# Performance work log

Hardware: AMD Instinct MI355X
Metric: run time of the kernel (lower is better)

## Reference

```python
import jax, jax.numpy as jnp
import numpy as np

DEPTH = 11  # tree depth -> depth+1 routing steps, n_nodes = 2**(DEPTH+1)-1 = 4095


def setup_inputs() -> dict:
    key = jax.random.key(0)
    k1, k2, k3 = jax.random.split(key, 3)
    B, D_in, D_out = 8192, 2048, 2048
    n_nodes = 2 ** (DEPTH + 1) - 1
    x = jax.random.normal(k1, (B, D_in), dtype=jnp.float32)
    # nn.Linear(input_width, n_nodes, bias=False).weight : (n_nodes, D_in)
    W_in = jax.random.normal(k2, (n_nodes, D_in), dtype=jnp.float32) / np.sqrt(D_in).astype(np.float32)
    # nn.Linear(n_nodes, output_width, bias=False).weight : (D_out, n_nodes)
    W_out = jax.random.normal(k3, (D_out, n_nodes), dtype=jnp.float32) / np.sqrt(n_nodes).astype(np.float32)
    return {"x": x, "W_in": W_in, "W_out": W_out}


def reference(x, W_in, W_out):
    B = x.shape[0]
    # Torch loop recomputes linear_in(x) every step; the result is identical each
    # iteration, so compute the (B, n_nodes) logits once and gather per depth step.
    logits_all = x @ W_in.T  # (B, n_nodes)

    def step(cur, _):
        # gather the logit of each sample's current tree node
        score = jnp.take_along_axis(logits_all, cur[:, None], axis=1)[:, 0]  # (B,)
        nxt = cur * 2 + (score >= 0).astype(jnp.int32) + 1  # left/right child
        return nxt, (cur, score)

    init = jnp.zeros((B,), dtype=jnp.int32)
    _, (nodes, scores) = jax.lax.scan(step, init, None, length=DEPTH + 1)
    nodes = nodes.T    # (B, depth+1) visited node ids
    scores = scores.T  # (B, depth+1) selected logits

    mlp1 = jax.nn.gelu(scores, approximate=False)  # exact GELU, matches nn.GELU
    # Conditional output projection: only the depth+1 visited columns of W_out
    # contribute per sample (FFF / conditional-MoE semantics).
    W_sel = W_out.T[nodes]  # (B, depth+1, D_out)
    return jnp.einsum('bd,bdo->bo', mlp1, W_sel)
```

## Files before the change

kernel.cpp:

```cpp
#include <hip/hip_runtime.h>
#include <math.h>

#define B_SZ     8192
#define D_IN     2048
#define D_OUT    2048
#define N_NODES  4095
#define STEPS    12
#define N_LEAVES 2048
#define N_SUB    512
#define CAP      64

typedef float f4_t __attribute__((ext_vector_type(4)));

__device__ __forceinline__ float4 nt_load4(const float* p) {
  f4_t v = __builtin_nontemporal_load((const f4_t*)p);
  return make_float4(v.x, v.y, v.z, v.w);
}
__device__ __forceinline__ void nt_store4(float* p, float4 v) {
  f4_t t; t.x = v.x; t.y = v.y; t.z = v.z; t.w = v.w;
  __builtin_nontemporal_store(t, (f4_t*)p);
}

__global__ __launch_bounds__(256) void transpose_wout(
    const float* __restrict__ W, float* __restrict__ Wt) {
  __shared__ float tile[64][65];
  const int bx = blockIdx.x;
  const int tid = threadIdx.x;
  const int col0 = (bx & 63) * 64;
  const int row0 = (bx >> 6) * 64;
  const int r  = tid >> 4;
  const int c4 = (tid & 15) * 4;

  #pragma unroll
  for (int i = 0; i < 4; ++i) {
    const int row = r + i * 16;
    const float* src = W + (size_t)(row0 + row) * N_NODES + col0 + c4;
    if (col0 + c4 + 3 < N_NODES) {
      const float4 v = nt_load4(src);
      tile[c4 + 0][row] = v.x; tile[c4 + 1][row] = v.y;
      tile[c4 + 2][row] = v.z; tile[c4 + 3][row] = v.w;
    } else {
      #pragma unroll
      for (int k = 0; k < 4; ++k)
        tile[c4 + k][row] = (col0 + c4 + k < N_NODES) ? src[k] : 0.0f;
    }
  }
  __syncthreads();
  #pragma unroll
  for (int i = 0; i < 4; ++i) {
    const int rn = r + i * 16;
    const int node = col0 + rn;
    if (node < N_NODES) {
      float4 v;
      v.x = tile[rn][c4 + 0]; v.y = tile[rn][c4 + 1];
      v.z = tile[rn][c4 + 2]; v.w = tile[rn][c4 + 3];
      *(float4*)(Wt + (size_t)node * D_OUT + row0 + c4) = v;
    }
  }
}

__global__ __launch_bounds__(256) void route_kernel(
    const float* __restrict__ x, const float* __restrict__ W_in,
    int* __restrict__ cnt, int* __restrict__ bucket,
    float* __restrict__ gsc) {
  const int wave = (int)((blockIdx.x * (size_t)blockDim.x + threadIdx.x) >> 6);
  const int lane = threadIdx.x & 63;
  if (wave >= B_SZ) return;

  const float* xbase = x + (size_t)wave * D_IN;
  float4 xv[8];
  #pragma unroll
  for (int i = 0; i < 8; ++i) xv[i] = nt_load4(xbase + (lane + i * 64) * 4);

  int cur = 0;
  #pragma unroll
  for (int d = 0; d < STEPS; ++d) {
    const float4* wr = (const float4*)(W_in + (size_t)cur * D_IN);
    float s = 0.0f;
    #pragma unroll
    for (int i = 0; i < 8; ++i) {
      const float4 w = wr[lane + i * 64];
      s += xv[i].x * w.x + xv[i].y * w.y + xv[i].z * w.z + xv[i].w * w.w;
    }
    #pragma unroll
    for (int off = 32; off > 0; off >>= 1) s += __shfl_xor(s, off);

    if (lane == 0) {
      gsc[wave * STEPS + d] = 0.5f * s * (1.0f + erff(s * 0.70710678118654752f));
      if (d == STEPS - 1) {
        const int leaf = cur - 2047;
        const int pos = atomicAdd(&cnt[leaf], 1);
        if (pos < CAP) bucket[leaf * CAP + pos] = wave;
      }
    }
    cur = cur * 2 + ((s >= 0.0f) ? 2 : 1);
  }
}

__global__ __launch_bounds__(256) void out_kernel(
    const float* __restrict__ Wt, const int* __restrict__ cnt,
    const int* __restrict__ bucket, const float* __restrict__ gsc,
    float* __restrict__ out) {
  const int sub = blockIdx.x * 4 + (threadIdx.x >> 6);
  const int lane = threadIdx.x & 63;
  const int col = blockIdx.y * 256 + lane * 4;

  int anc[10];
  {
    int nd = 511 + sub;
    #pragma unroll
    for (int d = 9; d >= 0; --d) { anc[d] = nd; nd = (nd - 1) >> 1; }
  }
  const int p10a = 1023 + 2 * sub;
  const int leaf0n = 2047 + 4 * sub;

  float4 wa[10], wp[2], wl[4];
  #pragma unroll
  for (int d = 0; d < 10; ++d)
    wa[d] = *(const float4*)(Wt + (size_t)anc[d] * D_OUT + col);
  #pragma unroll
  for (int k = 0; k < 2; ++k)
    wp[k] = *(const float4*)(Wt + (size_t)(p10a + k) * D_OUT + col);
  #pragma unroll
  for (int k = 0; k < 4; ++k)
    wl[k] = *(const float4*)(Wt + (size_t)(leaf0n + k) * D_OUT + col);

  int n0 = cnt[4 * sub + 0]; if (n0 > CAP) n0 = CAP;
  int n1 = cnt[4 * sub + 1]; if (n1 > CAP) n1 = CAP;
  int n2 = cnt[4 * sub + 2]; if (n2 > CAP) n2 = CAP;
  int n3 = cnt[4 * sub + 3]; if (n3 > CAP) n3 = CAP;
  const int p1 = n0, p2 = n0 + n1, p3 = n0 + n1 + n2;
  const int total = p3 + n3;

  for (int base = 0; base < total; base += 64) {
    const int m = (total - base < 64) ? (total - base) : 64;
    int packed = 0;
    {
      const int gi = base + lane;
      if (gi < total) {
        int lc, off;
        if      (gi < p1) { lc = 0; off = 0;  }
        else if (gi < p2) { lc = 1; off = p1; }
        else if (gi < p3) { lc = 2; off = p2; }
        else              { lc = 3; off = p3; }
        const int b = bucket[(4 * sub + lc) * CAP + (gi - off)];
        packed = (lc << 28) | b;
      }
    }
    int pA = __shfl(packed, 0);
    int pB = __shfl(packed, (m > 1) ? 1 : 0);
    const float4* gA = (const float4*)(gsc + (size_t)(pA & 0x0FFFFFFF) * STEPS);
    float4 a0 = gA[0], a1 = gA[1], a2 = gA[2];
    const float4* gB = (const float4*)(gsc + (size_t)(pB & 0x0FFFFFFF) * STEPS);
    float4 b0 = gB[0], b1 = gB[1], b2 = gB[2];

    for (int j = 0; j < m; ++j) {
      int jn = j + 2; if (jn >= m) jn = m - 1;
      const int pC = __shfl(packed, jn);
      const float4* gC = (const float4*)(gsc + (size_t)(pC & 0x0FFFFFFF) * STEPS);
      const float4 t0 = gC[0], t1 = gC[1], t2 = gC[2];

      const int b  = pA & 0x0FFFFFFF;
      const int lc = pA >> 28;
      const float4 w10 = (lc & 2) ? wp[1] : wp[0];
      const float4 w11 = (lc & 2) ? ((lc & 1) ? wl[3] : wl[2])
                                  : ((lc & 1) ? wl[1] : wl[0]);
      float4 acc;
      acc.x = a0.x * wa[0].x; acc.y = a0.x * wa[0].y;
      acc.z = a0.x * wa[0].z; acc.w = a0.x * wa[0].w;
      acc.x += a0.y * wa[1].x; acc.y += a0.y * wa[1].y;
      acc.z += a0.y * wa[1].z; acc.w += a0.y * wa[1].w;
      acc.x += a0.z * wa[2].x; acc.y += a0.z * wa[2].y;
      acc.z += a0.z * wa[2].z; acc.w += a0.z * wa[2].w;
      acc.x += a0.w * wa[3].x; acc.y += a0.w * wa[3].y;
      acc.z += a0.w * wa[3].z; acc.w += a0.w * wa[3].w;
      acc.x += a1.x * wa[4].x; acc.y += a1.x * wa[4].y;
      acc.z += a1.x * wa[4].z; acc.w += a1.x * wa[4].w;
      acc.x += a1.y * wa[5].x; acc.y += a1.y * wa[5].y;
      acc.z += a1.y * wa[5].z; acc.w += a1.y * wa[5].w;
      acc.x += a1.z * wa[6].x; acc.y += a1.z * wa[6].y;
      acc.z += a1.z * wa[6].z; acc.w += a1.z * wa[6].w;
      acc.x += a1.w * wa[7].x; acc.y += a1.w * wa[7].y;
      acc.z += a1.w * wa[7].z; acc.w += a1.w * wa[7].w;
      acc.x += a2.x * wa[8].x; acc.y += a2.x * wa[8].y;
      acc.z += a2.x * wa[8].z; acc.w += a2.x * wa[8].w;
      acc.x += a2.y * wa[9].x; acc.y += a2.y * wa[9].y;
      acc.z += a2.y * wa[9].z; acc.w += a2.y * wa[9].w;
      acc.x += a2.z * w10.x;   acc.y += a2.z * w10.y;
      acc.z += a2.z * w10.z;   acc.w += a2.z * w10.w;
      acc.x += a2.w * w11.x;   acc.y += a2.w * w11.y;
      acc.z += a2.w * w11.z;   acc.w += a2.w * w11.w;
      nt_store4(out + (size_t)b * D_OUT + col, acc);

      pA = pB; a0 = b0; a1 = b1; a2 = b2;
      pB = pC; b0 = t0; b1 = t1; b2 = t2;
    }
  }
}

extern "C" void kernel_launch(void* const* d_in, const int* in_sizes, int n_in,
                              void* d_out, int out_size, void* d_ws, size_t ws_size,
                              hipStream_t stream) {
  const float* x     = (const float*)d_in[0];
  const float* W_in  = (const float*)d_in[1];
  const float* W_out = (const float*)d_in[2];
  float* out = (float*)d_out;

  char* p = (char*)d_ws;
  float* Wt     = (float*)p;  p += (size_t)N_NODES * D_OUT * sizeof(float);
  int*   cnt    = (int*)p;    p += (size_t)N_LEAVES * sizeof(int);
  int*   bucket = (int*)p;    p += (size_t)N_LEAVES * CAP * sizeof(int);
  float* gsc    = (float*)p;

  hipMemsetAsync(cnt, 0, (size_t)N_LEAVES * sizeof(int), stream);

  route_kernel<<<dim3(B_SZ / 4), dim3(256), 0, stream>>>(
      x, W_in, cnt, bucket, gsc);

  transpose_wout<<<dim3(2048), dim3(256), 0, stream>>>(W_out, Wt);

  out_kernel<<<dim3(N_SUB / 4, 8), dim3(256), 0, stream>>>(
      Wt, cnt, bucket, gsc, out);
}
```

Measured before the change: 232.8 us.

## Split output kernel to one column per lane and hoist route weight loads

The output kernel now gives each lane one scalar column instead of a float4 and launches four times as many column blocks. This raises parallelism and cuts per-thread register pressure, but every sample's score row is reloaded by four times as many waves and stores become scalar. The routing kernel's loops are manually unrolled so all eight W_in float4 loads are issued before the dot product, exposing more memory-level parallelism per step.

```diff
diff --git a/kernel.cpp b/kernel.cpp
--- a/kernel.cpp
+++ b/kernel.cpp
@@ -15,10 +15,6 @@
 __device__ __forceinline__ float4 nt_load4(const float* p) {
   f4_t v = __builtin_nontemporal_load((const f4_t*)p);
   return make_float4(v.x, v.y, v.z, v.w);
-}
-__device__ __forceinline__ void nt_store4(float* p, float4 v) {
-  f4_t t; t.x = v.x; t.y = v.y; t.z = v.z; t.w = v.w;
-  __builtin_nontemporal_store(t, (f4_t*)p);
 }
 
 __global__ __launch_bounds__(256) void transpose_wout(
@@ -68,20 +64,37 @@
   if (wave >= B_SZ) return;
 
   const float* xbase = x + (size_t)wave * D_IN;
-  float4 xv[8];
-  #pragma unroll
-  for (int i = 0; i < 8; ++i) xv[i] = nt_load4(xbase + (lane + i * 64) * 4);
+  float4 xv0 = nt_load4(xbase + (lane + 0 * 64) * 4);
+  float4 xv1 = nt_load4(xbase + (lane + 1 * 64) * 4);
+  float4 xv2 = nt_load4(xbase + (lane + 2 * 64) * 4);
+  float4 xv3 = nt_load4(xbase + (lane + 3 * 64) * 4);
+  float4 xv4 = nt_load4(xbase + (lane + 4 * 64) * 4);
+  float4 xv5 = nt_load4(xbase + (lane + 5 * 64) * 4);
+  float4 xv6 = nt_load4(xbase + (lane + 6 * 64) * 4);
+  float4 xv7 = nt_load4(xbase + (lane + 7 * 64) * 4);
 
   int cur = 0;
   #pragma unroll
   for (int d = 0; d < STEPS; ++d) {
     const float4* wr = (const float4*)(W_in + (size_t)cur * D_IN);
+    const float4 w0 = wr[lane + 0 * 64];
+    const float4 w1 = wr[lane + 1 * 64];
+    const float4 w2 = wr[lane + 2 * 64];
+    const float4 w3 = wr[lane + 3 * 64];
+    const float4 w4 = wr[lane + 4 * 64];
+    const float4 w5 = wr[lane + 5 * 64];
+    const float4 w6 = wr[lane + 6 * 64];
+    const float4 w7 = wr[lane + 7 * 64];
     float s = 0.0f;
-    #pragma unroll
-    for (int i = 0; i < 8; ++i) {
-      const float4 w = wr[lane + i * 64];
-      s += xv[i].x * w.x + xv[i].y * w.y + xv[i].z * w.z + xv[i].w * w.w;
-    }
+    s += xv0.x * w0.x + xv0.y * w0.y + xv0.z * w0.z + xv0.w * w0.w;
+    s += xv1.x * w1.x + xv1.y * w1.y + xv1.z * w1.z + xv1.w * w1.w;
+    s += xv2.x * w2.x + xv2.y * w2.y + xv2.z * w2.z + xv2.w * w2.w;
+    s += xv3.x * w3.x + xv3.y * w3.y + xv3.z * w3.z + xv3.w * w3.w;
+    s += xv4.x * w4.x + xv4.y * w4.y + xv4.z * w4.z + xv4.w * w4.w;
+    s += xv5.x * w5.x + xv5.y * w5.y + xv5.z * w5.z + xv5.w * w5.w;
+    s += xv6.x * w6.x + xv6.y * w6.y + xv6.z * w6.z + xv6.w * w6.w;
+    s += xv7.x * w7.x + xv7.y * w7.y + xv7.z * w7.z + xv7.w * w7.w;
+
     #pragma unroll
     for (int off = 32; off > 0; off >>= 1) s += __shfl_xor(s, off);
 
@@ -103,7 +116,7 @@
     float* __restrict__ out) {
   const int sub = blockIdx.x * 4 + (threadIdx.x >> 6);
   const int lane = threadIdx.x & 63;
-  const int col = blockIdx.y * 256 + lane * 4;
+  const int col = blockIdx.y * 64 + lane;
 
   int anc[10];
   {
@@ -114,16 +127,16 @@
   const int p10a = 1023 + 2 * sub;
   const int leaf0n = 2047 + 4 * sub;
 
-  float4 wa[10], wp[2], wl[4];
+  float wa[10], wp[2], wl[4];
   #pragma unroll
   for (int d = 0; d < 10; ++d)
-    wa[d] = *(const float4*)(Wt + (size_t)anc[d] * D_OUT + col);
+    wa[d] = Wt[(size_t)anc[d] * D_OUT + col];
   #pragma unroll
   for (int k = 0; k < 2; ++k)
-    wp[k] = *(const float4*)(Wt + (size_t)(p10a + k) * D_OUT + col);
+    wp[k] = Wt[(size_t)(p10a + k) * D_OUT + col];
   #pragma unroll
   for (int k = 0; k < 4; ++k)
-    wl[k] = *(const float4*)(Wt + (size_t)(leaf0n + k) * D_OUT + col);
+    wl[k] = Wt[(size_t)(leaf0n + k) * D_OUT + col];
 
   int n0 = cnt[4 * sub + 0]; if (n0 > CAP) n0 = CAP;
   int n1 = cnt[4 * sub + 1]; if (n1 > CAP) n1 = CAP;
@@ -162,35 +175,23 @@
 
       const int b  = pA & 0x0FFFFFFF;
       const int lc = pA >> 28;
-      const float4 w10 = (lc & 2) ? wp[1] : wp[0];
-      const float4 w11 = (lc & 2) ? ((lc & 1) ? wl[3] : wl[2])
-                                  : ((lc & 1) ? wl[1] : wl[0]);
-      float4 acc;
-      acc.x = a0.x * wa[0].x; acc.y = a0.x * wa[0].y;
-      acc.z = a0.x * wa[0].z; acc.w = a0.x * wa[0].w;
-      acc.x += a0.y * wa[1].x; acc.y += a0.y * wa[1].y;
-      acc.z += a0.y * wa[1].z; acc.w += a0.y * wa[1].w;
-      acc.x += a0.z * wa[2].x; acc.y += a0.z * wa[2].y;
-      acc.z += a0.z * wa[2].z; acc.w += a0.z * wa[2].w;
-      acc.x += a0.w * wa[3].x; acc.y += a0.w * wa[3].y;
-      acc.z += a0.w * wa[3].z; acc.w += a0.w * wa[3].w;
-      acc.x += a1.x * wa[4].x; acc.y += a1.x * wa[4].y;
-      acc.z += a1.x * wa[4].z; acc.w += a1.x * wa[4].w;
-      acc.x += a1.y * wa[5].x; acc.y += a1.y * wa[5].y;
-      acc.z += a1.y * wa[5].z; acc.w += a1.y * wa[5].w;
-      acc.x += a1.z * wa[6].x; acc.y += a1.z * wa[6].y;
-      acc.z += a1.z * wa[6].z; acc.w += a1.z * wa[6].w;
-      acc.x += a1.w * wa[7].x; acc.y += a1.w * wa[7].y;
-      acc.z += a1.w * wa[7].z; acc.w += a1.w * wa[7].w;
-      acc.x += a2.x * wa[8].x; acc.y += a2.x * wa[8].y;
-      acc.z += a2.x * wa[8].z; acc.w += a2.x * wa[8].w;
-      acc.x += a2.y * wa[9].x; acc.y += a2.y * wa[9].y;
-      acc.z += a2.y * wa[9].z; acc.w += a2.y * wa[9].w;
-      acc.x += a2.z * w10.x;   acc.y += a2.z * w10.y;
-      acc.z += a2.z * w10.z;   acc.w += a2.z * w10.w;
-      acc.x += a2.w * w11.x;   acc.y += a2.w * w11.y;
-      acc.z += a2.w * w11.z;   acc.w += a2.w * w11.w;
-      nt_store4(out + (size_t)b * D_OUT + col, acc);
+      const float w10 = (lc & 2) ? wp[1] : wp[0];
+      const float w11 = (lc & 2) ? ((lc & 1) ? wl[3] : wl[2])
+                                 : ((lc & 1) ? wl[1] : wl[0]);
+      float acc;
+      acc  = a0.x * wa[0];
+      acc += a0.y * wa[1];
+      acc += a0.z * wa[2];
+      acc += a0.w * wa[3];
+      acc += a1.x * wa[4];
+      acc += a1.y * wa[5];
+      acc += a1.z * wa[6];
+      acc += a1.w * wa[7];
+      acc += a2.x * wa[8];
+      acc += a2.y * wa[9];
+      acc += a2.z * w10;
+      acc += a2.w * w11;
+      __builtin_nontemporal_store(acc, out + (size_t)b * D_OUT + col);
 
       pA = pB; a0 = b0; a1 = b1; a2 = b2;
       pB = pC; b0 = t0; b1 = t1; b2 = t2;
@@ -219,6 +220,6 @@
 
   transpose_wout<<<dim3(2048), dim3(256), 0, stream>>>(W_out, Wt);
 
-  out_kernel<<<dim3(N_SUB / 4, 8), dim3(256), 0, stream>>>(
+  out_kernel<<<dim3(N_SUB / 4, 32), dim3(256), 0, stream>>>(
       Wt, cnt, bucket, gsc, out);
 }
```

New measurement: 245.5 us. +5.4%, slower.
